# Kernel optimization log

Hardware: AMD Instinct MI355X
Metric: run time of the kernel (lower is better)

The kernel has to match this reference:

```python
import jax, jax.numpy as jnp
import numpy as np

D_MODEL = 1024
NUM_HEADS = 16
D_K = D_MODEL // NUM_HEADS

def setup_inputs() -> dict:
    key = jax.random.key(0)
    ks = jax.random.split(key, 8)
    B, S, D = 2, 2048, D_MODEL
    scale = 1.0 / np.sqrt(D)
    return {
        "X_q": jax.random.normal(ks[0], (B, S, D), dtype=jnp.float32),
        "X_k": jax.random.normal(ks[1], (B, S, D), dtype=jnp.float32),
        "X_v": jax.random.normal(ks[2], (B, S, D), dtype=jnp.float32),
        "W_q": jax.random.normal(ks[3], (D, D), dtype=jnp.float32) * scale,
        "W_k": jax.random.normal(ks[4], (D, D), dtype=jnp.float32) * scale,
        "W_v": jax.random.normal(ks[5], (D, D), dtype=jnp.float32) * scale,
        "W_o": jax.random.normal(ks[6], (D, D), dtype=jnp.float32) * scale,
        "b_o": jnp.zeros((D,), dtype=jnp.float32),
    }

def reference(X_q, X_k, X_v, W_q, W_k, W_v, W_o, b_o):
    B, S, D = X_q.shape
    H, dk = NUM_HEADS, D_K
    # nn.Linear: x @ W.T
    Q = (X_q @ W_q.T).reshape(B, H, S, dk)  # faithful raw view, no transpose
    K = (X_k @ W_k.T).reshape(B, H, S, dk)
    V = (X_v @ W_v.T).reshape(B, H, S, dk)
    A = jnp.einsum("bhqd,bhkd->bhqk", Q, K) / np.sqrt(dk)  # [B,H,S,S]
    A = jax.nn.softmax(A, axis=-1)
    H_cat = jnp.einsum("bhqk,bhkd->bhqd", A, V).reshape(B, S, D)
    return H_cat @ W_o.T + b_o
```

## Files before the change

### kernel.cpp

```cpp
#include <hip/hip_runtime.h>

typedef __bf16 bf16;
typedef bf16 bf16x8 __attribute__((ext_vector_type(8)));
typedef bf16 bf16x4 __attribute__((ext_vector_type(4)));
typedef bf16 bf16x2 __attribute__((ext_vector_type(2)));
typedef float f32x4 __attribute__((ext_vector_type(4)));
typedef float f32x16 __attribute__((ext_vector_type(16)));
typedef int i32x4 __attribute__((ext_vector_type(4)));

#define XSZ 4194304
#define WSZ 1048576
#define KDIM 1024
#define QSCALE 0.1803368801111137f

__device__ __forceinline__ void async16(const bf16* g, bf16* l) {
  __builtin_amdgcn_global_load_lds(
      (const __attribute__((address_space(1))) unsigned int*)g,
      (__attribute__((address_space(3))) unsigned int*)l, 16, 0, 0);
}

__device__ __forceinline__ bf16x8 ld16(const bf16* p) {
  return __builtin_bit_cast(bf16x8, *(const i32x4*)p);
}

__device__ __forceinline__ f32x4 mfma16(bf16x8 a, bf16x8 b, f32x4 c) {
  return __builtin_amdgcn_mfma_f32_16x16x32_bf16(a, b, c, 0, 0, 0);
}
__device__ __forceinline__ f32x16 mfma32(bf16x8 a, bf16x8 b, f32x16 c) {
  return __builtin_amdgcn_mfma_f32_32x32x16_bf16(a, b, c, 0, 0, 0);
}

__device__ __forceinline__ int packbf2(float lo, float hi) {
  bf16x2 t; t[0] = (bf16)lo; t[1] = (bf16)hi;
  return __builtin_bit_cast(int, t);
}

__device__ __forceinline__ float fast_exp2(float x) {
#if __has_builtin(__builtin_amdgcn_exp2f)
  return __builtin_amdgcn_exp2f(x);
#else
  return exp2f(x);
#endif
}


__global__ __launch_bounds__(256) void cast_all(const float* __restrict__ Xq, const float* __restrict__ Xk,
                                                const float* __restrict__ Xv, const float* __restrict__ Wq,
                                                const float* __restrict__ Wk, const float* __restrict__ Wv,
                                                const float* __restrict__ Wo, bf16* __restrict__ dst) {
  size_t i = ((size_t)blockIdx.x * 256 + threadIdx.x) * 8;
  const float* src; size_t off; float scale = 1.0f;
  if (i < XSZ)                { src = Xq; off = i; }
  else if (i < 2 * (size_t)XSZ) { src = Xk; off = i - XSZ; }
  else if (i < 3 * (size_t)XSZ) { src = Xv; off = i - 2 * (size_t)XSZ; }
  else if (i < 3 * (size_t)XSZ + WSZ) { src = Wq; off = i - 3 * (size_t)XSZ; scale = QSCALE; }
  else if (i < 3 * (size_t)XSZ + 2 * (size_t)WSZ) { src = Wk; off = i - 3 * (size_t)XSZ - WSZ; }
  else if (i < 3 * (size_t)XSZ + 3 * (size_t)WSZ) { src = Wv; off = i - 3 * (size_t)XSZ - 2 * (size_t)WSZ; }
  else                        { src = Wo; off = i - 3 * (size_t)XSZ - 3 * (size_t)WSZ; }
  float4 a = *(const float4*)(src + off);
  float4 b = *(const float4*)(src + off + 4);
  bf16x8 o;
  o[0] = (bf16)(a.x * scale); o[1] = (bf16)(a.y * scale);
  o[2] = (bf16)(a.z * scale); o[3] = (bf16)(a.w * scale);
  o[4] = (bf16)(b.x * scale); o[5] = (bf16)(b.y * scale);
  o[6] = (bf16)(b.z * scale); o[7] = (bf16)(b.w * scale);
  *(bf16x8*)(dst + i) = o;
}

__device__ __forceinline__ void gemm_nt_core(const bf16* __restrict__ A, const bf16* __restrict__ Bm,
                                             int m0, int n0, bf16* lds, f32x4 acc[4][4]) {
  const int t = threadIdx.x;
  const int lane = t & 63, wave = t >> 6;
  const int wm = wave & 1, wn = wave >> 1;
  const int quad = lane >> 4, m16 = lane & 15;
  const bf16* gA[2]; int dstc[2];
  #pragma unroll
  for (int j = 0; j < 2; j++) {
    int c = t + j * 256;
    int row = c >> 2;
    int col = ((c & 3) ^ (row & 3)) * 8;
    gA[j] = A + (size_t)(m0 + row) * KDIM + col;
    dstc[j] = c * 8;
  }
  const ptrdiff_t dBA = (Bm + (size_t)n0 * KDIM) - (A + (size_t)m0 * KDIM);
  const int swzA = quad ^ (m16 & 3);
  #pragma unroll
  for (int j = 0; j < 2; j++) {
    async16(gA[j], lds + dstc[j]);
    async16(gA[j] + dBA, lds + 4096 + dstc[j]);
  }
  for (int kt = 0; kt < 32; ++kt) {
    __syncthreads();
    const int cur = (kt & 1) * 8192;
    if (kt + 1 < 32) {
      const int nxt = 8192 - cur;
      #pragma unroll
      for (int j = 0; j < 2; j++) {
        async16(gA[j] + (kt + 1) * 32, lds + nxt + dstc[j]);
        async16(gA[j] + dBA + (kt + 1) * 32, lds + nxt + 4096 + dstc[j]);
      }
    }
    const bf16* As = lds + cur;
    const bf16* Bs = As + 4096;
    bf16x8 af[4], bfv[4];
    #pragma unroll
    for (int i = 0; i < 4; i++)
      af[i] = ld16(As + (wm * 64 + i * 16 + m16) * 32 + swzA * 8);
    #pragma unroll
    for (int i = 0; i < 4; i++)
      bfv[i] = ld16(Bs + (wn * 64 + i * 16 + m16) * 32 + swzA * 8);
    #pragma unroll
    for (int mi = 0; mi < 4; mi++)
      #pragma unroll
      for (int ni = 0; ni < 4; ni++)
        acc[mi][ni] = mfma16(af[mi], bfv[ni], acc[mi][ni]);
  }
}

__global__ __launch_bounds__(256, 3) void proj_gemm(const bf16* __restrict__ xq, const bf16* __restrict__ xk,
                                                 const bf16* __restrict__ xv, const bf16* __restrict__ wq,
                                                 const bf16* __restrict__ wk, const bf16* __restrict__ wv,
                                                 bf16* __restrict__ Qo, bf16* __restrict__ Ko,
                                                 bf16* __restrict__ Vo) {
  __shared__ __align__(16) bf16 lds[2 * 8192];
  const int z = blockIdx.z;
  const bf16* A = (z == 0) ? xq : (z == 1) ? xk : xv;
  const bf16* W = (z == 0) ? wq : (z == 1) ? wk : wv;
  bf16* C = (z == 0) ? Qo : (z == 1) ? Ko : Vo;
  f32x4 acc[4][4];
  #pragma unroll
  for (int i = 0; i < 4; i++)
    #pragma unroll
    for (int j = 0; j < 4; j++) acc[i][j] = (f32x4){0.f, 0.f, 0.f, 0.f};
  gemm_nt_core(A, W, blockIdx.y * 128, blockIdx.x * 128, lds, acc);
  const int lane = threadIdx.x & 63, wave = threadIdx.x >> 6;
  const int wm = wave & 1, wn = wave >> 1, quad = lane >> 4, m16 = lane & 15;
  const int row0 = blockIdx.y * 128 + wm * 64;
  const int col0 = blockIdx.x * 128 + wn * 64;
  #pragma unroll
  for (int mi = 0; mi < 4; mi++)
    #pragma unroll
    for (int ni = 0; ni < 4; ni++)
      #pragma unroll
      for (int r = 0; r < 4; r++) {
        int row = row0 + mi * 16 + quad * 4 + r;
        int col = col0 + ni * 16 + m16;
        C[(size_t)row * 1024 + col] = (bf16)acc[mi][ni][r];
      }
}

__global__ __launch_bounds__(256, 3) void out_gemm(const bf16* __restrict__ Hm, const bf16* __restrict__ wo,
                                                const float* __restrict__ bias, float* __restrict__ out) {
  __shared__ __align__(16) bf16 lds[2 * 6144];
  const int t = threadIdx.x;
  const int lane = t & 63, wave = t >> 6;
  const int wm = wave & 1, wn = wave >> 1;
  const int quad = lane >> 4, m16 = lane & 15;
  const int m0 = blockIdx.y * 128, n0 = blockIdx.x * 64;
  const bf16* gA[2]; int dstA[2];
  #pragma unroll
  for (int j = 0; j < 2; j++) {
    int c = t + j * 256;
    int row = c >> 2;
    int col = ((c & 3) ^ (row & 3)) * 8;
    gA[j] = Hm + (size_t)(m0 + row) * KDIM + col;
    dstA[j] = c * 8;
  }
  const bf16* gB; int dstB;
  {
    int c = t;
    int row = c >> 2;
    int col = ((c & 3) ^ (row & 3)) * 8;
    gB = wo + (size_t)(n0 + row) * KDIM + col;
    dstB = c * 8;
  }
  const int swzA = quad ^ (m16 & 3);
  f32x4 acc[4][2];
  #pragma unroll
  for (int i = 0; i < 4; i++)
    #pragma unroll
    for (int j = 0; j < 2; j++) acc[i][j] = (f32x4){0.f, 0.f, 0.f, 0.f};
  #pragma unroll
  for (int j = 0; j < 2; j++) async16(gA[j], lds + dstA[j]);
  async16(gB, lds + 4096 + dstB);
  for (int kt = 0; kt < 32; ++kt) {
    __syncthreads();
    const int cur = (kt & 1) * 6144;
    if (kt + 1 < 32) {
      const int nxt = 6144 - cur;
      #pragma unroll
      for (int j = 0; j < 2; j++) async16(gA[j] + (kt + 1) * 32, lds + nxt + dstA[j]);
      async16(gB + (kt + 1) * 32, lds + nxt + 4096 + dstB);
    }
    const bf16* As = lds + cur;
    const bf16* Bs = As + 4096;
    bf16x8 af[4], bfv[2];
    #pragma unroll
    for (int i = 0; i < 4; i++)
      af[i] = ld16(As + (wm * 64 + i * 16 + m16) * 32 + swzA * 8);
    #pragma unroll
    for (int i = 0; i < 2; i++)
      bfv[i] = ld16(Bs + (wn * 32 + i * 16 + m16) * 32 + swzA * 8);
    #pragma unroll
    for (int mi = 0; mi < 4; mi++)
      #pragma unroll
      for (int ni = 0; ni < 2; ni++)
        acc[mi][ni] = mfma16(af[mi], bfv[ni], acc[mi][ni]);
  }
  const int row0 = m0 + wm * 64;
  const int col0 = n0 + wn * 32;
  float bv[2];
  #pragma unroll
  for (int ni = 0; ni < 2; ni++) bv[ni] = bias[col0 + ni * 16 + m16];
  #pragma unroll
  for (int mi = 0; mi < 4; mi++)
    #pragma unroll
    for (int ni = 0; ni < 2; ni++)
      #pragma unroll
      for (int r = 0; r < 4; r++) {
        int row = row0 + mi * 16 + quad * 4 + r;
        int col = col0 + ni * 16 + m16;
        out[(size_t)row * 1024 + col] = acc[mi][ni][r] + bv[ni];
      }
}

__global__ __launch_bounds__(256) void transpose_v(const bf16* __restrict__ V, bf16* __restrict__ Vt) {
  __shared__ bf16 T[64 * 65];
  const int t = threadIdx.x;
  const bf16* src = V + (size_t)blockIdx.y * (2048 * 64) + (size_t)blockIdx.x * 64 * 64;
  bf16* dst = Vt + (size_t)blockIdx.y * (2048 * 64) + (size_t)blockIdx.x * 64;
  #pragma unroll
  for (int j = 0; j < 2; j++) {
    int c = t + j * 256;
    int row = c >> 3, col8 = (c & 7) * 8;
    bf16x8 v = *(const bf16x8*)(src + row * 64 + col8);
    #pragma unroll
    for (int i = 0; i < 8; i++) T[row * 65 + col8 + i] = v[i];
  }
  __syncthreads();
  #pragma unroll
  for (int j = 0; j < 2; j++) {
    int c = t + j * 256;
    int d = c >> 3, k8 = (c & 7) * 8;
    bf16x8 o;
    #pragma unroll
    for (int i = 0; i < 8; i++) o[i] = T[(k8 + i) * 65 + d];
    *(bf16x8*)(dst + (size_t)d * 2048 + k8) = o;
  }
}

__global__ __launch_bounds__(512, 2) void attn_kernel(const bf16* __restrict__ Qg,
                                                      const bf16* __restrict__ Kg,
                                                      const bf16* __restrict__ Vtg,
                                                      bf16* __restrict__ Hout) {
  __shared__ __align__(16) bf16 smem[32768];
  const int t = threadIdx.x;
  const int lane = t & 63;
  const int w = (t >> 6) & 3;
  const int half = t >> 8;
  const int tt = t & 255;
  const int l31 = lane & 31, h = lane >> 5, l7 = lane & 7;
  bf16* hb = smem + half * 16384;
  const int L = blockIdx.x + 16 * blockIdx.y;
  const int xcd = L & 7, j5 = L >> 3;
  const int bh = xcd * 4 + (j5 & 3);
  const int qt = j5 >> 2;
  const size_t base = (size_t)bh * (2048 * 64);
  const bf16* Kp = Kg + base;
  const bf16* Vp = Vtg + base;
  const int q = qt * 128 + w * 32 + l31;

  bf16x8 qf[4];
  #pragma unroll
  for (int kc = 0; kc < 4; kc++)
    qf[kc] = *(const bf16x8*)(Qg + base + (size_t)q * 64 + 16 * kc + 8 * h);

  f32x16 oacc[2];
  #pragma unroll
  for (int mt = 0; mt < 2; mt++)
    #pragma unroll
    for (int i = 0; i < 16; i++) oacc[mt][i] = 0.f;
  float lrow = 0.f;

  const bf16* ksrc[2]; const bf16* vsrc[2]; int dstc[2];
  #pragma unroll
  for (int j = 0; j < 2; j++) {
    int c = tt + j * 256;
    int row = c >> 3;
    int sw = ((c & 7) ^ (row & 7)) * 8;
    ksrc[j] = Kp + (size_t)(half * 1024 + row) * 64 + sw;
    vsrc[j] = Vp + (size_t)row * 2048 + half * 1024 + sw;
    dstc[j] = c * 8;
  }

  #pragma unroll
  for (int j = 0; j < 2; j++) {
    async16(ksrc[j], hb + dstc[j]);
    async16(vsrc[j], hb + 4096 + dstc[j]);
  }

  for (int st = 0; st < 16; ++st) {
    __syncthreads();
    const int buf = st & 1;
    if (st + 1 < 16) {
      const int nb = (buf ^ 1) * 8192;
      #pragma unroll
      for (int j = 0; j < 2; j++) {
        async16(ksrc[j] + (st + 1) * 4096, hb + nb + dstc[j]);
        async16(vsrc[j] + (st + 1) * 64,   hb + nb + 4096 + dstc[j]);
      }
    }
    bf16* Kb = hb + buf * 8192;
    bf16* Vb = Kb + 4096;

    #pragma unroll
    for (int mtq = 0; mtq < 2; mtq++) {
      f32x16 sacc;
      #pragma unroll
      for (int i = 0; i < 16; i++) sacc[i] = 0.f;
      #pragma unroll
      for (int kc = 0; kc < 4; kc++) {
        bf16x8 kf = ld16(Kb + (32 * mtq + l31) * 64 + (((2 * kc + h) ^ l7) << 3));
        sacc = mfma32(kf, qf[kc], sacc);
      }
      int pd[8];
      float sum = 0.f;
      #pragma unroll
      for (int p = 0; p < 8; p++) {
        float p0 = fast_exp2(sacc[2 * p]);
        float p1 = fast_exp2(sacc[2 * p + 1]);
        sum += p0 + p1;
        pd[p] = packbf2(p0, p1);
      }
      lrow += sum;
      #pragma unroll
      for (int c1 = 0; c1 < 2; c1++) {
        const int kcp = 2 * mtq + c1;
        const int rro = 2 * c1 + h;
        const int rrp = 2 * c1 + 1 - h;
        int s0 = __shfl_xor(pd[2 * rrp], 32, 64);
        int s1 = __shfl_xor(pd[2 * rrp + 1], 32, 64);
        int o0 = pd[2 * rro], o1 = pd[2 * rro + 1];
        i32x4 w4;
        w4.x = h ? s0 : o0;
        w4.y = h ? s1 : o1;
        w4.z = h ? o0 : s0;
        w4.w = h ? o1 : s1;
        bf16x8 pfrag = __builtin_bit_cast(bf16x8, w4);
        #pragma unroll
        for (int mtd = 0; mtd < 2; mtd++) {
          bf16x8 vf = ld16(Vb + (32 * mtd + l31) * 64 + (((2 * kcp + h) ^ l7) << 3));
          oacc[mtd] = mfma32(vf, pfrag, oacc[mtd]);
        }
      }
    }
  }
  __syncthreads();

  lrow += __shfl_xor(lrow, 32, 64);
  float* Sf = (float*)smem;
  float* Tf = Sf + w * 2048;
  float* Lb = Sf + 8192 + w * 32;
  if (half) {
    #pragma unroll
    for (int mt = 0; mt < 2; mt++)
      #pragma unroll
      for (int r = 0; r < 16; r++) {
        int d = 32 * mt + (r & 3) + 8 * (r >> 2) + 4 * h;
        Tf[d * 32 + l31] = oacc[mt][r];
      }
    if (!h) Lb[l31] = lrow;
  }
  __syncthreads();
  if (!half) {
    float linv = 1.f / (lrow + Lb[l31]);
    #pragma unroll
    for (int mt = 0; mt < 2; mt++)
      #pragma unroll
      for (int r = 0; r < 16; r++) {
        int d = 32 * mt + (r & 3) + 8 * (r >> 2) + 4 * h;
        Tf[d * 32 + l31] = (oacc[mt][r] + Tf[d * 32 + l31]) * linv;
      }
  }
  __syncthreads();
  bf16* Hq = Hout + base + (size_t)(qt * 128 + w * 32 + l31) * 64 + 32 * h;
  #pragma unroll
  for (int s = 0; s < 2; s++) {
    int se = half * 2 + s;
    bf16x8 o;
    #pragma unroll
    for (int i = 0; i < 8; i++) o[i] = (bf16)Tf[(32 * h + se * 8 + i) * 32 + l31];
    *(bf16x8*)(Hq + se * 8) = o;
  }
}

extern "C" void kernel_launch(void* const* d_in, const int* in_sizes, int n_in,
                              void* d_out, int out_size, void* d_ws, size_t ws_size,
                              hipStream_t stream) {
  const float* Xq = (const float*)d_in[0];
  const float* Xk = (const float*)d_in[1];
  const float* Xv = (const float*)d_in[2];
  const float* Wq = (const float*)d_in[3];
  const float* Wk = (const float*)d_in[4];
  const float* Wv = (const float*)d_in[5];
  const float* Wo = (const float*)d_in[6];
  const float* bo = (const float*)d_in[7];

  bf16* ws = (bf16*)d_ws;
  bf16* xq = ws;
  bf16* xk = ws + XSZ;
  bf16* xv = ws + 2 * (size_t)XSZ;
  bf16* wq = ws + 3 * (size_t)XSZ;
  bf16* wk = wq + WSZ;
  bf16* wv = wk + WSZ;
  bf16* wo = wv + WSZ;
  bf16* q  = wo + WSZ;
  bf16* k  = q + XSZ;
  bf16* v  = k + XSZ;
  bf16* vt = xv;
  bf16* h  = xq;

  cast_all<<<8192, 256, 0, stream>>>(Xq, Xk, Xv, Wq, Wk, Wv, Wo, ws);
  proj_gemm<<<dim3(8, 32, 3), 256, 0, stream>>>(xq, xk, xv, wq, wk, wv, q, k, v);
  transpose_v<<<dim3(32, 32), 256, 0, stream>>>(v, vt);
  attn_kernel<<<dim3(16, 32), 512, 0, stream>>>(q, k, vt, h);
  out_gemm<<<dim3(16, 32), 256, 0, stream>>>(h, wo, bo, (float*)d_out);
}
```

Baseline: 230.8 us.

## Replace async LDS loads with register-staged prefetch and padded LDS rows

```diff
diff --git a/kernel.cpp b/kernel.cpp
--- a/kernel.cpp
+++ b/kernel.cpp
@@ -21,6 +21,17 @@
 
 __device__ __forceinline__ bf16x8 ld16(const bf16* p) {
   return __builtin_bit_cast(bf16x8, *(const i32x4*)p);
+}
+
+__device__ __forceinline__ bf16x8 ld8(const bf16* p) {
+  bf16x4 lo = *(const bf16x4*)p;
+  bf16x4 hi = *(const bf16x4*)(p + 4);
+  return __builtin_shufflevector(lo, hi, 0, 1, 2, 3, 4, 5, 6, 7);
+}
+
+__device__ __forceinline__ void st8s(bf16* p, bf16x8 v) {
+  *(bf16x4*)p       = __builtin_shufflevector(v, v, 0, 1, 2, 3);
+  *(bf16x4*)(p + 4) = __builtin_shufflevector(v, v, 4, 5, 6, 7);
 }
 
 __device__ __forceinline__ f32x4 mfma16(bf16x8 a, bf16x8 b, f32x4 c) {
@@ -249,18 +260,22 @@
   }
 }
 
+#define KS2 68
+#define SUBT (64 * KS2)
+#define BUFSZ (2 * SUBT)
+#define HALFSZ (2 * BUFSZ)
 __global__ __launch_bounds__(512, 2) void attn_kernel(const bf16* __restrict__ Qg,
                                                       const bf16* __restrict__ Kg,
                                                       const bf16* __restrict__ Vtg,
                                                       bf16* __restrict__ Hout) {
-  __shared__ __align__(16) bf16 smem[32768];
+  __shared__ __align__(16) bf16 smem[2 * HALFSZ];
   const int t = threadIdx.x;
   const int lane = t & 63;
   const int w = (t >> 6) & 3;
   const int half = t >> 8;
   const int tt = t & 255;
-  const int l31 = lane & 31, h = lane >> 5, l7 = lane & 7;
-  bf16* hb = smem + half * 16384;
+  const int l31 = lane & 31, h = lane >> 5;
+  bf16* hb = smem + half * HALFSZ;
   const int L = blockIdx.x + 16 * blockIdx.y;
   const int xcd = L & 7, j5 = L >> 3;
   const int bh = xcd * 4 + (j5 & 3);
@@ -282,36 +297,53 @@
     for (int i = 0; i < 16; i++) oacc[mt][i] = 0.f;
   float lrow = 0.f;
 
-  const bf16* ksrc[2]; const bf16* vsrc[2]; int dstc[2];
+  const bf16* ksrc[2]; const bf16* vsrc[2]; int ldst[2];
   #pragma unroll
   for (int j = 0; j < 2; j++) {
     int c = tt + j * 256;
     int row = c >> 3;
-    int sw = ((c & 7) ^ (row & 7)) * 8;
-    ksrc[j] = Kp + (size_t)(half * 1024 + row) * 64 + sw;
-    vsrc[j] = Vp + (size_t)row * 2048 + half * 1024 + sw;
-    dstc[j] = c * 8;
-  }
-
-  #pragma unroll
-  for (int j = 0; j < 2; j++) {
-    async16(ksrc[j], hb + dstc[j]);
-    async16(vsrc[j], hb + 4096 + dstc[j]);
+    int col8 = (c & 7) * 8;
+    ksrc[j] = Kp + (size_t)(half * 1024 + row) * 64 + col8;
+    vsrc[j] = Vp + (size_t)row * 2048 + half * 1024 + col8;
+    ldst[j] = row * KS2 + col8;
+  }
+
+  bf16x8 kreg[2], vreg[2];
+  #pragma unroll
+  for (int j = 0; j < 2; j++) {
+    kreg[j] = *(const bf16x8*)(ksrc[j]);
+    vreg[j] = *(const bf16x8*)(vsrc[j]);
+  }
+  #pragma unroll
+  for (int j = 0; j < 2; j++) {
+    st8s(hb + ldst[j], kreg[j]);
+    st8s(hb + SUBT + ldst[j], vreg[j]);
+  }
+  #pragma unroll
+  for (int j = 0; j < 2; j++) {
+    kreg[j] = *(const bf16x8*)(ksrc[j] + 4096);
+    vreg[j] = *(const bf16x8*)(vsrc[j] + 64);
   }
 
   for (int st = 0; st < 16; ++st) {
     __syncthreads();
-    const int buf = st & 1;
+    const bf16* Kb = hb + (st & 1) * BUFSZ;
+    const bf16* Vb = Kb + SUBT;
     if (st + 1 < 16) {
-      const int nb = (buf ^ 1) * 8192;
+      bf16* nb = hb + ((st & 1) ^ 1) * BUFSZ;
       #pragma unroll
       for (int j = 0; j < 2; j++) {
-        async16(ksrc[j] + (st + 1) * 4096, hb + nb + dstc[j]);
-        async16(vsrc[j] + (st + 1) * 64,   hb + nb + 4096 + dstc[j]);
+        st8s(nb + ldst[j], kreg[j]);
+        st8s(nb + SUBT + ldst[j], vreg[j]);
       }
     }
-    bf16* Kb = hb + buf * 8192;
-    bf16* Vb = Kb + 4096;
+    if (st + 2 < 16) {
+      #pragma unroll
+      for (int j = 0; j < 2; j++) {
+        kreg[j] = *(const bf16x8*)(ksrc[j] + (size_t)(st + 2) * 4096);
+        vreg[j] = *(const bf16x8*)(vsrc[j] + (size_t)(st + 2) * 64);
+      }
+    }
 
     #pragma unroll
     for (int mtq = 0; mtq < 2; mtq++) {
@@ -320,7 +352,7 @@
       for (int i = 0; i < 16; i++) sacc[i] = 0.f;
       #pragma unroll
       for (int kc = 0; kc < 4; kc++) {
-        bf16x8 kf = ld16(Kb + (32 * mtq + l31) * 64 + (((2 * kc + h) ^ l7) << 3));
+        bf16x8 kf = ld8(Kb + (32 * mtq + l31) * KS2 + 16 * kc + 8 * h);
         sacc = mfma32(kf, qf[kc], sacc);
       }
       int pd[8];
@@ -349,7 +381,7 @@
         bf16x8 pfrag = __builtin_bit_cast(bf16x8, w4);
         #pragma unroll
         for (int mtd = 0; mtd < 2; mtd++) {
-          bf16x8 vf = ld16(Vb + (32 * mtd + l31) * 64 + (((2 * kcp + h) ^ l7) << 3));
+          bf16x8 vf = ld8(Vb + (32 * mtd + l31) * KS2 + 16 * kcp + 8 * h);
           oacc[mtd] = mfma32(vf, pfrag, oacc[mtd]);
         }
       }
```

After: 244.9 us. 1.06x slower.
